# Optimization experiments

Hardware: AMD Instinct MI355X
Metric: run time of the kernel (lower is better)

## Reference

```python
import jax, jax.numpy as jnp
import numpy as np

B, N, D, H = 2, 2048, 1024, 16
DK = D // H  # 64


def setup_inputs() -> dict:
    key = jax.random.key(0)
    k0, k1, k2, k3, k4 = jax.random.split(key, 5)
    x = jax.random.normal(k0, (B, N, D), jnp.float32)
    # per-head kqv Linear weights, stored input-major: y = x @ Wkqv[h] + bkqv[h]
    Wkqv = jax.random.normal(k1, (H, D, 3 * DK), jnp.float32) / np.float32(np.sqrt(D))
    bkqv = jax.random.normal(k2, (H, 3 * DK), jnp.float32) * 0.01
    Wproj = jax.random.normal(k3, (D, D), jnp.float32) / np.float32(np.sqrt(D))
    bproj = jax.random.normal(k4, (D,), jnp.float32) * 0.01
    return {"x": x, "Wkqv": Wkqv, "bkqv": bkqv, "Wproj": Wproj, "bproj": bproj}


def reference(x, Wkqv, bkqv, Wproj, bproj):
    Bb, Nn, Dd = x.shape
    Hh, _, three_dk = Wkqv.shape
    dk = three_dk // 3
    # all-head kqv projection: [B, H, N, 3*dk]
    p = jnp.einsum('bnd,hde->bhne', x, Wkqv) + bkqv[None, :, None, :]
    # torch views (B,N,dk,3) and splits last dim -> interleaved columns
    p = p.reshape(Bb, Hh, Nn, dk, 3)
    k, q, v = p[..., 0], p[..., 1], p[..., 2]
    # NOTE: original computes attention_scores(k, q) = K @ Q^T / sqrt(dk)
    scores = jnp.einsum('bhnd,bhmd->bhnm', k, q) / jnp.sqrt(jnp.asarray(dk, x.dtype))
    causal = jnp.tril(jnp.ones((Nn, Nn), bool))  # buffer mask[-N:, -N:]
    scores = jnp.where(causal[None, None], scores, -jnp.inf)
    attn = jax.nn.softmax(scores, axis=-1)
    sa = jnp.einsum('bhnm,bhmd->bhnd', attn, v)  # [B,H,N,dk]
    sa = sa.transpose(0, 2, 1, 3).reshape(Bb, Nn, Dd)  # concat heads along feature
    return sa @ Wproj + bproj
```

## Files before the change

### kernel.cpp

```cpp
#include <hip/hip_runtime.h>
#include <hip/hip_bf16.h>


typedef __bf16 bf16x8 __attribute__((ext_vector_type(8)));
typedef float f32x4 __attribute__((ext_vector_type(4)));
typedef float f32x16 __attribute__((ext_vector_type(16)));

#define MFMA_BF16 __builtin_amdgcn_mfma_f32_16x16x32_bf16
#define MFMA32 __builtin_amdgcn_mfma_f32_32x32x16_bf16

static __device__ __forceinline__ unsigned cvtpk(float lo, float hi) {
    unsigned r;
    asm("v_cvt_pk_bf16_f32 %0, %1, %2" : "=v"(r) : "v"(lo), "v"(hi));
    return r;
}

static __device__ __forceinline__ void gld16(const void* g, void* l) {
    __builtin_amdgcn_global_load_lds(
        (const __attribute__((address_space(1))) unsigned int*)g,
        (__attribute__((address_space(3))) unsigned int*)l, 16, 0, 0);
}


__global__ __launch_bounds__(256) void cvt_f32_bf16(const float* __restrict__ in,
                                                    __hip_bfloat16* __restrict__ out) {
    int i = (blockIdx.x * 256 + threadIdx.x) * 4;
    float4 v = *(const float4*)&in[i];
    struct alignas(8) bh4 { __hip_bfloat16 a, b, c, d; };
    bh4 r{__float2bfloat16(v.x), __float2bfloat16(v.y),
          __float2bfloat16(v.z), __float2bfloat16(v.w)};
    *(bh4*)&out[i] = r;
}

__global__ __launch_bounds__(256) void transpose_cvt(const float* __restrict__ in,
                                                     __hip_bfloat16* __restrict__ out,
                                                     int R, int C) {
    __shared__ float tile[32][33];
    int b = blockIdx.z;
    int r0 = blockIdx.y * 32, c0 = blockIdx.x * 32;
    int tx = threadIdx.x, ty = threadIdx.y;
    const float* ip = in + (size_t)b * R * C;
    __hip_bfloat16* op = out + (size_t)b * R * C;
#pragma unroll
    for (int j = 0; j < 32; j += 8)
        tile[ty + j][tx] = ip[(size_t)(r0 + ty + j) * C + (c0 + tx)];
    __syncthreads();
#pragma unroll
    for (int j = 0; j < 32; j += 8)
        op[(size_t)(c0 + ty + j) * R + (r0 + tx)] = __float2bfloat16(tile[tx][ty + j]);
}

__global__ __launch_bounds__(512) void gemm_qkv(const __hip_bfloat16* __restrict__ Ag,
                                                const __hip_bfloat16* __restrict__ Btg,
                                                const float* __restrict__ bias,
                                                __hip_bfloat16* __restrict__ Kf,
                                                __hip_bfloat16* __restrict__ Qf,
                                                __hip_bfloat16* __restrict__ Vf) {
    __shared__ __hip_bfloat16 smem[57344];
    const int t = threadIdx.x;
    const int lane = t & 63, wid = t >> 6;
    const int wm = wid >> 2, wn = wid & 3;
    const int h = blockIdx.x;
    const int row0 = blockIdx.y * 256;
    const int col0 = h * 192;
    const int lr = lane & 15, lg = lane >> 4;
    const int g_r = lane >> 3;
    const int g_s8 = ((lane & 7) ^ g_r) * 8;
    const int sw0 = ((lg) ^ (lr & 7)) * 8;
    const int sw1 = ((4 + lg) ^ (lr & 7)) * 8;

#define STAGE_QKV(buf, kt)                                                            \
    do {                                                                              \
        const int k0_ = (kt) * 64;                                                    \
        __hip_bfloat16* Ad_ = smem + (buf) * 16384;                                   \
        __hip_bfloat16* Bd_ = smem + 32768 + (buf) * 12288;                           \
        _Pragma("unroll") for (int r_ = 0; r_ < 4; ++r_) {                            \
            const int grp_ = r_ * 8 + wid;                                            \
            gld16(&Ag[(size_t)(row0 + grp_ * 8 + g_r) * 1024 + k0_ + g_s8],           \
                  Ad_ + grp_ * 512);                                                  \
        }                                                                             \
        _Pragma("unroll") for (int r_ = 0; r_ < 3; ++r_) {                            \
            const int grp_ = r_ * 8 + wid;                                            \
            gld16(&Btg[(size_t)(col0 + grp_ * 8 + g_r) * 1024 + k0_ + g_s8],          \
                  Bd_ + grp_ * 512);                                                  \
        }                                                                             \
    } while (0)

    f32x4 acc[8][3] = {};

    STAGE_QKV(0, 0);
    STAGE_QKV(1, 1);
    asm volatile("s_waitcnt vmcnt(7)" ::: "memory");
    __builtin_amdgcn_sched_barrier(0);
    __builtin_amdgcn_s_barrier();
    __builtin_amdgcn_sched_barrier(0);

    int cur = 0;
    for (int kt = 0; kt < 16; ++kt) {
        const __hip_bfloat16* Ab = smem + cur * 16384;
        const __hip_bfloat16* Bb = smem + 32768 + cur * 12288;
        bf16x8 af[8], bf[3];
#pragma unroll
        for (int j = 0; j < 3; ++j)
            bf[j] = *(const bf16x8*)&Bb[(wn * 48 + j * 16 + lr) * 64 + sw0];
#pragma unroll
        for (int i = 0; i < 8; ++i)
            af[i] = *(const bf16x8*)&Ab[(wm * 128 + i * 16 + lr) * 64 + sw0];
        __builtin_amdgcn_s_setprio(1);
#pragma unroll
        for (int i = 0; i < 8; ++i)
#pragma unroll
            for (int j = 0; j < 3; ++j)
                acc[i][j] = MFMA_BF16(af[i], bf[j], acc[i][j], 0, 0, 0);
        __builtin_amdgcn_s_setprio(0);
#pragma unroll
        for (int j = 0; j < 3; ++j)
            bf[j] = *(const bf16x8*)&Bb[(wn * 48 + j * 16 + lr) * 64 + sw1];
#pragma unroll
        for (int i = 0; i < 8; ++i)
            af[i] = *(const bf16x8*)&Ab[(wm * 128 + i * 16 + lr) * 64 + sw1];
        asm volatile("s_waitcnt lgkmcnt(0)" ::: "memory");
        __builtin_amdgcn_sched_barrier(0);
        __builtin_amdgcn_s_barrier();
        __builtin_amdgcn_sched_barrier(0);
        if (kt + 2 < 16) STAGE_QKV(cur, kt + 2);
        __builtin_amdgcn_s_setprio(1);
#pragma unroll
        for (int i = 0; i < 8; ++i)
#pragma unroll
            for (int j = 0; j < 3; ++j)
                acc[i][j] = MFMA_BF16(af[i], bf[j], acc[i][j], 0, 0, 0);
        __builtin_amdgcn_s_setprio(0);
        if (kt <= 13) {
            asm volatile("s_waitcnt vmcnt(7)" ::: "memory");
        } else {
            asm volatile("s_waitcnt vmcnt(0)" ::: "memory");
        }
        __builtin_amdgcn_sched_barrier(0);
        __builtin_amdgcn_s_barrier();
        __builtin_amdgcn_sched_barrier(0);
        cur ^= 1;
    }
#undef STAGE_QKV

    const int b = row0 >> 11, n_base = row0 & 2047, bh = b * 16 + h;
    __hip_bfloat16 (*tile)[204] = (__hip_bfloat16 (*)[204])smem;
#pragma unroll
    for (int i = 0; i < 8; ++i)
#pragma unroll
        for (int j = 0; j < 3; ++j)
#pragma unroll
            for (int r = 0; r < 4; ++r) {
                int trow = wm * 128 + i * 16 + lg * 4 + r;
                int tcol = wn * 48 + j * 16 + lr;
                float v = acc[i][j][r] + bias[col0 + tcol];
                if (tcol % 3 == 0) v *= 0.125f;
                tile[trow][tcol] = __float2bfloat16(v);
            }
    __syncthreads();
#pragma unroll
    for (int k = 0; k < 4; ++k) {
        const int c = t + 512 * k;
        const int l = c & 63, lo = l & 31, hi = l >> 5;
        {
            const int dc = (c >> 6) & 3, so = c >> 8;
            ushort u[8];
#pragma unroll
            for (int i = 0; i < 8; ++i)
                u[i] = *(const ushort*)&tile[so * 32 + lo][3 * (dc * 16 + 8 * hi + i)];
            *(uint4*)&Kf[(((size_t)bh * 64 + (n_base >> 5) + so) * 4 + dc) * 512 + l * 8] =
                *(const uint4*)u;
        }
        {
            const int dc = (c >> 6) & 3, sub = (c >> 8) & 1, mt_off = c >> 9;
            ushort u[8];
#pragma unroll
            for (int i = 0; i < 8; ++i)
                u[i] = *(const ushort*)&tile[mt_off * 64 + sub * 32 + lo]
                                           [3 * (dc * 16 + 8 * hi + i) + 1];
            *(uint4*)&Qf[((((size_t)bh * 32 + (n_base >> 6) + mt_off) * 2 + sub) * 4 + dc) * 512 +
                         l * 8] = *(const uint4*)u;
        }
        {
            const int accN = (c >> 6) & 1, kc = (c >> 7) & 3, mt_off = c >> 9;
            ushort u[8];
#pragma unroll
            for (int i = 0; i < 8; ++i)
                u[i] = *(const ushort*)&tile[mt_off * 64 + kc * 16 + 8 * hi + i]
                                           [3 * (accN * 32 + lo) + 2];
            *(uint4*)&Vf[((((size_t)bh * 32 + (n_base >> 6) + mt_off) * 4 + kc) * 2 + accN) * 512 +
                         l * 8] = *(const uint4*)u;
        }
    }
}

__global__ __launch_bounds__(256, 3) void attn_fwd(const __hip_bfloat16* __restrict__ Kf,
                                                   const __hip_bfloat16* __restrict__ Qf,
                                                   const __hip_bfloat16* __restrict__ Vf,
                                                   __hip_bfloat16* __restrict__ sa) {
    __shared__ float mbuf[3][64][35];
    __shared__ __hip_bfloat16 ot[32][66];
    const int id = blockIdx.x;
    const int xcd = id & 7, qq = id >> 3;
    const int bh = xcd * 4 + (qq & 3);
    const int slice = 63 - (qq >> 2);
    const int t = threadIdx.x, lane = t & 63, wid = t >> 6;
    const int col = lane & 31, half = lane >> 5;
    const int par = wid;
    const int n0 = slice * 32;

    const __hip_bfloat16* Kfp = Kf + (size_t)bh * 131072;
    const __hip_bfloat16* Qfp = Qf + (size_t)bh * 131072;
    const __hip_bfloat16* Vfp = Vf + (size_t)bh * 131072;

    bf16x8 kf[4];
#pragma unroll
    for (int dc = 0; dc < 4; ++dc)
        kf[dc] = *(const bf16x8*)&Kfp[((size_t)slice * 4 + dc) * 512 + lane * 8];

    f32x16 acc0 = {}, acc1 = {};
    float m_run = -3.0e29f, l_run = 0.f;
    const int ng = n0 + col;
    const int T = (n0 + 95) >> 6;

    bf16x8 qa[4], qb[4];
    if (par < T) {
#pragma unroll
        for (int dc = 0; dc < 4; ++dc) {
            qa[dc] = *(const bf16x8*)&Qfp[(((size_t)par * 2 + 0) * 4 + dc) * 512 + lane * 8];
            qb[dc] = *(const bf16x8*)&Qfp[(((size_t)par * 2 + 1) * 4 + dc) * 512 + lane * 8];
        }
    }

    for (int j = par; j < T; j += 4) {
        const int m0 = j << 6;
        bf16x8 va[4], vb[4];
#pragma unroll
        for (int kc = 0; kc < 4; ++kc) {
            va[kc] = *(const bf16x8*)&Vfp[(((size_t)j * 4 + kc) * 2 + 0) * 512 + lane * 8];
            vb[kc] = *(const bf16x8*)&Vfp[(((size_t)j * 4 + kc) * 2 + 1) * 512 + lane * 8];
        }
        f32x16 s0 = {}, s1 = {};
        __builtin_amdgcn_s_setprio(1);
#pragma unroll
        for (int dc = 0; dc < 4; ++dc) s0 = MFMA32(qa[dc], kf[dc], s0, 0, 0, 0);
#pragma unroll
        for (int dc = 0; dc < 4; ++dc) s1 = MFMA32(qb[dc], kf[dc], s1, 0, 0, 0);
        __builtin_amdgcn_s_setprio(0);
        if (j + 4 < T) {
#pragma unroll
            for (int dc = 0; dc < 4; ++dc) {
                qa[dc] = *(const bf16x8*)&Qfp[(((size_t)(j + 4) * 2 + 0) * 4 + dc) * 512 + lane * 8];
                qb[dc] = *(const bf16x8*)&Qfp[(((size_t)(j + 4) * 2 + 1) * 4 + dc) * 512 + lane * 8];
            }
        }
        if (m0 + 63 > n0) {
            const int mb = m0 + 4 * half;
#pragma unroll
            for (int r = 0; r < 16; ++r) {
                int mg = mb + (r & 3) + 8 * (r >> 2);
                if (mg > ng)      s0[r] = -1e30f;
                if (mg + 32 > ng) s1[r] = -1e30f;
            }
        }
        float mx = s0[0];
#pragma unroll
        for (int r = 1; r < 16; ++r) mx = fmaxf(mx, s0[r]);
#pragma unroll
        for (int r = 0; r < 16; ++r) mx = fmaxf(mx, s1[r]);
        mx = fmaxf(mx, __shfl_xor(mx, 32));
        float nm = fmaxf(m_run, mx);
        float scale = __expf(m_run - nm);
        m_run = nm;
        float rs = 0.f;
#pragma unroll
        for (int r = 0; r < 16; ++r) { s0[r] = __expf(s0[r] - nm); rs += s0[r]; }
#pragma unroll
        for (int r = 0; r < 16; ++r) { s1[r] = __expf(s1[r] - nm); rs += s1[r]; }
        rs += __shfl_xor(rs, 32);
        l_run = l_run * scale + rs;
        acc0 *= scale;
        acc1 *= scale;

#pragma unroll
        for (int kc = 0; kc < 4; ++kc) {
            float p0, p1, p2, p3, p4, p5, p6, p7;
            if (kc == 0)      { p0=s0[0]; p1=s0[1]; p2=s0[2]; p3=s0[3]; p4=s0[4]; p5=s0[5]; p6=s0[6]; p7=s0[7]; }
            else if (kc == 1) { p0=s0[8]; p1=s0[9]; p2=s0[10]; p3=s0[11]; p4=s0[12]; p5=s0[13]; p6=s0[14]; p7=s0[15]; }
            else if (kc == 2) { p0=s1[0]; p1=s1[1]; p2=s1[2]; p3=s1[3]; p4=s1[4]; p5=s1[5]; p6=s1[6]; p7=s1[7]; }
            else              { p0=s1[8]; p1=s1[9]; p2=s1[10]; p3=s1[11]; p4=s1[12]; p5=s1[13]; p6=s1[14]; p7=s1[15]; }
            unsigned a0 = cvtpk(p0, p1), a1 = cvtpk(p2, p3);
            unsigned a2 = cvtpk(p4, p5), a3 = cvtpk(p6, p7);
            unsigned t0 = __shfl_xor(a0, 32), t1 = __shfl_xor(a1, 32);
            unsigned t2 = __shfl_xor(a2, 32), t3 = __shfl_xor(a3, 32);
            union { unsigned u[4]; bf16x8 v; } pb;
            pb.u[0] = half ? t2 : a0;
            pb.u[1] = half ? t3 : a1;
            pb.u[2] = half ? a2 : t0;
            pb.u[3] = half ? a3 : t1;
            __builtin_amdgcn_s_setprio(1);
            acc0 = MFMA32(va[kc], pb.v, acc0, 0, 0, 0);
            acc1 = MFMA32(vb[kc], pb.v, acc1, 0, 0, 0);
            __builtin_amdgcn_s_setprio(0);
        }
    }

    if (wid) {
#pragma unroll
        for (int r = 0; r < 16; ++r) {
            mbuf[wid - 1][lane][r]      = acc0[r];
            mbuf[wid - 1][lane][16 + r] = acc1[r];
        }
        mbuf[wid - 1][lane][32] = m_run;
        mbuf[wid - 1][lane][33] = l_run;
    }
    __syncthreads();
    if (!wid) {
#pragma unroll
        for (int w = 0; w < 3; ++w) {
            float mB = mbuf[w][lane][32], lB = mbuf[w][lane][33];
            float nm = fmaxf(m_run, mB);
            float sA = __expf(m_run - nm), sB = __expf(mB - nm);
            m_run = nm;
            l_run = l_run * sA + lB * sB;
#pragma unroll
            for (int r = 0; r < 16; ++r) {
                acc0[r] = acc0[r] * sA + mbuf[w][lane][r] * sB;
                acc1[r] = acc1[r] * sA + mbuf[w][lane][16 + r] * sB;
            }
        }
        float inv = 1.0f / l_run;
#pragma unroll
        for (int r = 0; r < 16; ++r) {
            int d0 = (r & 3) + 8 * (r >> 2) + 4 * half;
            ot[col][d0]      = __float2bfloat16(acc0[r] * inv);
            ot[col][32 + d0] = __float2bfloat16(acc1[r] * inv);
        }
        const int b = bh >> 4, h = bh & 15;
#pragma unroll
        for (int tt = 0; tt < 16; ++tt) {
            int rrow = tt * 2 + half;
            unsigned v = *(const unsigned*)&ot[rrow][col * 2];
            *(unsigned*)&sa[((size_t)(b * 2048 + n0 + rrow)) * 1024 + h * 64 + col * 2] = v;
        }
    }
}

__global__ __launch_bounds__(256) void gemm_proj(const __hip_bfloat16* __restrict__ Ag,
                                                 const __hip_bfloat16* __restrict__ Btg,
                                                 const float* __restrict__ bias,
                                                 float* __restrict__ out) {
    __shared__ __hip_bfloat16 smem[32768];
    const int t = threadIdx.x;
    const int lane = t & 63, wid = t >> 6;
    const int wm = wid >> 1, wn = wid & 1;
    const int row0 = blockIdx.y * 128, col0 = blockIdx.x * 128;
    const int lr = lane & 15, lg = lane >> 4;
    const int g_r = lane >> 3;
    const int g_s8 = ((lane & 7) ^ g_r) * 8;
    const int sw0 = ((lg) ^ (lr & 7)) * 8;
    const int sw1 = ((4 + lg) ^ (lr & 7)) * 8;

#define STAGE_PROJ(buf, kt)                                                           \
    do {                                                                              \
        const int k0_ = (kt) * 64;                                                    \
        __hip_bfloat16* Ad_ = smem + (buf) * 8192;                                    \
        __hip_bfloat16* Bd_ = smem + 16384 + (buf) * 8192;                            \
        _Pragma("unroll") for (int r_ = 0; r_ < 4; ++r_) {                            \
            const int grp_ = r_ * 4 + wid;                                            \
            gld16(&Ag[(size_t)(row0 + grp_ * 8 + g_r) * 1024 + k0_ + g_s8],           \
                  Ad_ + grp_ * 512);                                                  \
            gld16(&Btg[(size_t)(col0 + grp_ * 8 + g_r) * 1024 + k0_ + g_s8],          \
                  Bd_ + grp_ * 512);                                                  \
        }                                                                             \
    } while (0)

    f32x4 acc[4][4] = {};

    STAGE_PROJ(0, 0);
    STAGE_PROJ(1, 1);
    asm volatile("s_waitcnt vmcnt(8)" ::: "memory");
    __builtin_amdgcn_sched_barrier(0);
    __builtin_amdgcn_s_barrier();
    __builtin_amdgcn_sched_barrier(0);

    int cur = 0;
    for (int kt = 0; kt < 16; ++kt) {
        const __hip_bfloat16* Ab = smem + cur * 8192;
        const __hip_bfloat16* Bb = smem + 16384 + cur * 8192;
        bf16x8 af[4], bf[4];
#pragma unroll
        for (int j = 0; j < 4; ++j)
            bf[j] = *(const bf16x8*)&Bb[(wn * 64 + j * 16 + lr) * 64 + sw0];
#pragma unroll
        for (int i = 0; i < 4; ++i)
            af[i] = *(const bf16x8*)&Ab[(wm * 64 + i * 16 + lr) * 64 + sw0];
        __builtin_amdgcn_s_setprio(1);
#pragma unroll
        for (int i = 0; i < 4; ++i)
#pragma unroll
            for (int j = 0; j < 4; ++j)
                acc[i][j] = MFMA_BF16(af[i], bf[j], acc[i][j], 0, 0, 0);
        __builtin_amdgcn_s_setprio(0);
#pragma unroll
        for (int j = 0; j < 4; ++j)
            bf[j] = *(const bf16x8*)&Bb[(wn * 64 + j * 16 + lr) * 64 + sw1];
#pragma unroll
        for (int i = 0; i < 4; ++i)
            af[i] = *(const bf16x8*)&Ab[(wm * 64 + i * 16 + lr) * 64 + sw1];
        asm volatile("s_waitcnt lgkmcnt(0)" ::: "memory");
        __builtin_amdgcn_sched_barrier(0);
        __builtin_amdgcn_s_barrier();
        __builtin_amdgcn_sched_barrier(0);
        if (kt + 2 < 16) STAGE_PROJ(cur, kt + 2);
        __builtin_amdgcn_s_setprio(1);
#pragma unroll
        for (int i = 0; i < 4; ++i)
#pragma unroll
            for (int j = 0; j < 4; ++j)
                acc[i][j] = MFMA_BF16(af[i], bf[j], acc[i][j], 0, 0, 0);
        __builtin_amdgcn_s_setprio(0);
        if (kt <= 13) {
            asm volatile("s_waitcnt vmcnt(8)" ::: "memory");
        } else {
            asm volatile("s_waitcnt vmcnt(0)" ::: "memory");
        }
        __builtin_amdgcn_sched_barrier(0);
        __builtin_amdgcn_s_barrier();
        __builtin_amdgcn_sched_barrier(0);
        cur ^= 1;
    }
#undef STAGE_PROJ

#pragma unroll
    for (int i = 0; i < 4; ++i)
#pragma unroll
        for (int j = 0; j < 4; ++j)
#pragma unroll
            for (int r = 0; r < 4; ++r) {
                int rg = row0 + wm * 64 + i * 16 + lg * 4 + r;
                int cg = col0 + wn * 64 + j * 16 + lr;
                out[(size_t)rg * 1024 + cg] = acc[i][j][r] + bias[cg];
            }
}

extern "C" void kernel_launch(void* const* d_in, const int* in_sizes, int n_in,
                              void* d_out, int out_size, void* d_ws, size_t ws_size,
                              hipStream_t stream) {
    const float* x     = (const float*)d_in[0];
    const float* Wkqv  = (const float*)d_in[1];
    const float* bkqv  = (const float*)d_in[2];
    const float* Wproj = (const float*)d_in[3];
    const float* bproj = (const float*)d_in[4];

    char* w = (char*)d_ws;
    __hip_bfloat16* xb  = (__hip_bfloat16*)(w + 0);
    __hip_bfloat16* sab = (__hip_bfloat16*)(w + 0);
    __hip_bfloat16* Wt  = (__hip_bfloat16*)(w + 8388608);
    __hip_bfloat16* Kf  = (__hip_bfloat16*)(w + 16777216);
    __hip_bfloat16* Qf  = (__hip_bfloat16*)(w + 25165824);
    __hip_bfloat16* Vf  = (__hip_bfloat16*)(w + 33554432);
    __hip_bfloat16* WpT = (__hip_bfloat16*)(w + 41943040);
    if (ws_size < 50331648) return;

    cvt_f32_bf16<<<4096, 256, 0, stream>>>(x, xb);
    transpose_cvt<<<dim3(6, 32, 16), dim3(32, 8), 0, stream>>>(Wkqv, Wt, 1024, 192);
    gemm_qkv<<<dim3(16, 16), 512, 0, stream>>>(xb, Wt, bkqv, Kf, Qf, Vf);
    transpose_cvt<<<dim3(32, 32, 1), dim3(32, 8), 0, stream>>>(Wproj, WpT, 1024, 1024);
    attn_fwd<<<2048, 256, 0, stream>>>(Kf, Qf, Vf, sab);
    gemm_proj<<<dim3(8, 32), 256, 0, stream>>>(sab, WpT, bproj, (float*)d_out);
}
```

Before: 99.42 us.

## Fold log2e into K scale, seed MFMA with -m, lazy softmax rescale

Folds log2(e)/sqrt(dk) into the K projection scale so the softmax can use exp2 directly. The running max is subtracted by seeding the MFMA accumulator with -m_run. The max and sum reductions become tree reductions. Rescaling of the accumulators is skipped unless some block maximum exceeds the running max by more than a threshold of 8. This removes per-element subtracts, serial reduction chains and per-tile accumulator multiplies, at the cost of letting exponentials grow up to 2^8 before renormalisation, which is a precision risk, and of relying on an initial max of -64.

```diff
diff --git a/kernel.cpp b/kernel.cpp
--- a/kernel.cpp
+++ b/kernel.cpp
@@ -154,7 +154,7 @@
                 int trow = wm * 128 + i * 16 + lg * 4 + r;
                 int tcol = wn * 48 + j * 16 + lr;
                 float v = acc[i][j][r] + bias[col0 + tcol];
-                if (tcol % 3 == 0) v *= 0.125f;
+                if (tcol % 3 == 0) v *= 0.18033688f;
                 tile[trow][tcol] = __float2bfloat16(v);
             }
     __syncthreads();
@@ -219,7 +219,7 @@
         kf[dc] = *(const bf16x8*)&Kfp[((size_t)slice * 4 + dc) * 512 + lane * 8];
 
     f32x16 acc0 = {}, acc1 = {};
-    float m_run = -3.0e29f, l_run = 0.f;
+    float m_run = -64.0f, l_run = 0.f;
     const int ng = n0 + col;
     const int T = (n0 + 95) >> 6;
 
@@ -240,7 +240,10 @@
             va[kc] = *(const bf16x8*)&Vfp[(((size_t)j * 4 + kc) * 2 + 0) * 512 + lane * 8];
             vb[kc] = *(const bf16x8*)&Vfp[(((size_t)j * 4 + kc) * 2 + 1) * 512 + lane * 8];
         }
-        f32x16 s0 = {}, s1 = {};
+        f32x16 s0, s1;
+        const float negm = -m_run;
+#pragma unroll
+        for (int r = 0; r < 16; ++r) { s0[r] = negm; s1[r] = negm; }
         __builtin_amdgcn_s_setprio(1);
 #pragma unroll
         for (int dc = 0; dc < 4; ++dc) s0 = MFMA32(qa[dc], kf[dc], s0, 0, 0, 0);
@@ -263,24 +266,38 @@
                 if (mg + 32 > ng) s1[r] = -1e30f;
             }
         }
-        float mx = s0[0];
-#pragma unroll
-        for (int r = 1; r < 16; ++r) mx = fmaxf(mx, s0[r]);
-#pragma unroll
-        for (int r = 0; r < 16; ++r) mx = fmaxf(mx, s1[r]);
-        mx = fmaxf(mx, __shfl_xor(mx, 32));
-        float nm = fmaxf(m_run, mx);
-        float scale = __expf(m_run - nm);
-        m_run = nm;
-        float rs = 0.f;
-#pragma unroll
-        for (int r = 0; r < 16; ++r) { s0[r] = __expf(s0[r] - nm); rs += s0[r]; }
-#pragma unroll
-        for (int r = 0; r < 16; ++r) { s1[r] = __expf(s1[r] - nm); rs += s1[r]; }
-        rs += __shfl_xor(rs, 32);
-        l_run = l_run * scale + rs;
-        acc0 *= scale;
-        acc1 *= scale;
+        float mxt[16];
+#pragma unroll
+        for (int r = 0; r < 16; ++r) mxt[r] = fmaxf(s0[r], s1[r]);
+#pragma unroll
+        for (int off = 8; off; off >>= 1)
+#pragma unroll
+            for (int r = 0; r < off; ++r) mxt[r] = fmaxf(mxt[r], mxt[r + off]);
+        float mx = fmaxf(mxt[0], __shfl_xor(mxt[0], 32));
+        if (__all(mx <= 8.0f)) {
+#pragma unroll
+            for (int r = 0; r < 16; ++r) { s0[r] = exp2f(s0[r]); s1[r] = exp2f(s1[r]); }
+        } else {
+            float mxp = fmaxf(mx, 0.0f);
+            float sc = exp2f(-mxp);
+            m_run += mxp;
+            l_run *= sc;
+#pragma unroll
+            for (int r = 0; r < 16; ++r) {
+                s0[r] = exp2f(s0[r] - mxp);
+                s1[r] = exp2f(s1[r] - mxp);
+                acc0[r] *= sc;
+                acc1[r] *= sc;
+            }
+        }
+        float rst[16];
+#pragma unroll
+        for (int r = 0; r < 16; ++r) rst[r] = s0[r] + s1[r];
+#pragma unroll
+        for (int off = 8; off; off >>= 1)
+#pragma unroll
+            for (int r = 0; r < off; ++r) rst[r] += rst[r + off];
+        l_run += rst[0] + __shfl_xor(rst[0], 32);
 
 #pragma unroll
         for (int kc = 0; kc < 4; ++kc) {
@@ -320,7 +337,7 @@
         for (int w = 0; w < 3; ++w) {
             float mB = mbuf[w][lane][32], lB = mbuf[w][lane][33];
             float nm = fmaxf(m_run, mB);
-            float sA = __expf(m_run - nm), sB = __expf(mB - nm);
+            float sA = exp2f(m_run - nm), sB = exp2f(mB - nm);
             m_run = nm;
             l_run = l_run * sA + lB * sB;
 #pragma unroll
```

New measurement: 251.2 us. 2.53x slower.

## Merge prep kernels and give each attention wave its own query slice

Applied to the files above, without the earlier changes.

The x conversion and both weight transpose-converts become one launch that dispatches on block index, removing two kernel launches. The attention kernel now assigns four adjacent 32-row query slices (a band) to the four waves of one block. Each wave walks the full key range alone, and the waves stay in lockstep with a barrier so they share key/value loads in cache. This removes the cross-wave LDS merge of partial softmax states and cuts the grid from 2048 blocks to 512. In exchange each wave does serial work along the whole sequence, waves with smaller slices do redundant masked iterations up to the band maximum, and there is less parallelism per output row.

```diff
diff --git a/kernel.cpp b/kernel.cpp
--- a/kernel.cpp
+++ b/kernel.cpp
@@ -21,33 +21,48 @@
         (__attribute__((address_space(3))) unsigned int*)l, 16, 0, 0);
 }
 
-
-__global__ __launch_bounds__(256) void cvt_f32_bf16(const float* __restrict__ in,
-                                                    __hip_bfloat16* __restrict__ out) {
-    int i = (blockIdx.x * 256 + threadIdx.x) * 4;
-    float4 v = *(const float4*)&in[i];
-    struct alignas(8) bh4 { __hip_bfloat16 a, b, c, d; };
-    bh4 r{__float2bfloat16(v.x), __float2bfloat16(v.y),
-          __float2bfloat16(v.z), __float2bfloat16(v.w)};
-    *(bh4*)&out[i] = r;
-}
-
-__global__ __launch_bounds__(256) void transpose_cvt(const float* __restrict__ in,
-                                                     __hip_bfloat16* __restrict__ out,
-                                                     int R, int C) {
+__global__ __launch_bounds__(256) void prep(const float* __restrict__ x,
+                                            const float* __restrict__ Wkqv,
+                                            const float* __restrict__ Wproj,
+                                            __hip_bfloat16* __restrict__ xb,
+                                            __hip_bfloat16* __restrict__ Wt,
+                                            __hip_bfloat16* __restrict__ WpT) {
     __shared__ float tile[32][33];
-    int b = blockIdx.z;
-    int r0 = blockIdx.y * 32, c0 = blockIdx.x * 32;
-    int tx = threadIdx.x, ty = threadIdx.y;
-    const float* ip = in + (size_t)b * R * C;
-    __hip_bfloat16* op = out + (size_t)b * R * C;
+    const int bid = blockIdx.x, t = threadIdx.x;
+    if (bid < 4096) {
+        int i = (bid * 256 + t) * 4;
+        float4 v = *(const float4*)&x[i];
+        struct alignas(8) bh4 { __hip_bfloat16 a, b, c, d; };
+        bh4 r{__float2bfloat16(v.x), __float2bfloat16(v.y),
+              __float2bfloat16(v.z), __float2bfloat16(v.w)};
+        *(bh4*)&xb[i] = r;
+        return;
+    }
+    const int tx = t & 31, ty = t >> 5;
+    const float* in;
+    __hip_bfloat16* out;
+    int R, C, r0, c0;
+    if (bid < 7168) {
+        int r = bid - 4096;
+        int bz = r / 192, rem = r % 192, by = rem / 6, bx = rem % 6;
+        R = 1024; C = 192;
+        in = Wkqv + (size_t)bz * R * C;
+        out = Wt + (size_t)bz * R * C;
+        r0 = by * 32; c0 = bx * 32;
+    } else {
+        int r = bid - 7168;
+        int by = r / 32, bx = r % 32;
+        R = 1024; C = 1024;
+        in = Wproj; out = WpT;
+        r0 = by * 32; c0 = bx * 32;
+    }
 #pragma unroll
     for (int j = 0; j < 32; j += 8)
-        tile[ty + j][tx] = ip[(size_t)(r0 + ty + j) * C + (c0 + tx)];
+        tile[ty + j][tx] = in[(size_t)(r0 + ty + j) * C + (c0 + tx)];
     __syncthreads();
 #pragma unroll
     for (int j = 0; j < 32; j += 8)
-        op[(size_t)(c0 + ty + j) * R + (r0 + tx)] = __float2bfloat16(tile[tx][ty + j]);
+        out[(size_t)(c0 + ty + j) * R + (r0 + tx)] = __float2bfloat16(tile[tx][ty + j]);
 }
 
 __global__ __launch_bounds__(512) void gemm_qkv(const __hip_bfloat16* __restrict__ Ag,
@@ -198,16 +213,17 @@
                                                    const __hip_bfloat16* __restrict__ Qf,
                                                    const __hip_bfloat16* __restrict__ Vf,
                                                    __hip_bfloat16* __restrict__ sa) {
-    __shared__ float mbuf[3][64][35];
-    __shared__ __hip_bfloat16 ot[32][66];
+    __shared__ __hip_bfloat16 ot[4][32][66];
     const int id = blockIdx.x;
-    const int xcd = id & 7, qq = id >> 3;
-    const int bh = xcd * 4 + (qq & 3);
-    const int slice = 63 - (qq >> 2);
+    const int xcd = id & 7, q = id >> 3;
+    const int bh = xcd * 4 + (q & 3);
+    const int band = 15 - (q >> 2);
     const int t = threadIdx.x, lane = t & 63, wid = t >> 6;
     const int col = lane & 31, half = lane >> 5;
-    const int par = wid;
+    const int slice = band * 4 + wid;
     const int n0 = slice * 32;
+    const int ng = n0 + col;
+    const int Tmax = 2 * band + 2;
 
     const __hip_bfloat16* Kfp = Kf + (size_t)bh * 131072;
     const __hip_bfloat16* Qfp = Qf + (size_t)bh * 131072;
@@ -220,19 +236,16 @@
 
     f32x16 acc0 = {}, acc1 = {};
     float m_run = -3.0e29f, l_run = 0.f;
-    const int ng = n0 + col;
-    const int T = (n0 + 95) >> 6;
 
     bf16x8 qa[4], qb[4];
-    if (par < T) {
-#pragma unroll
-        for (int dc = 0; dc < 4; ++dc) {
-            qa[dc] = *(const bf16x8*)&Qfp[(((size_t)par * 2 + 0) * 4 + dc) * 512 + lane * 8];
-            qb[dc] = *(const bf16x8*)&Qfp[(((size_t)par * 2 + 1) * 4 + dc) * 512 + lane * 8];
-        }
-    }
-
-    for (int j = par; j < T; j += 4) {
+#pragma unroll
+    for (int dc = 0; dc < 4; ++dc) {
+        qa[dc] = *(const bf16x8*)&Qfp[((size_t)0 * 4 + dc) * 512 + lane * 8];
+        qb[dc] = *(const bf16x8*)&Qfp[((size_t)1 * 4 + dc) * 512 + lane * 8];
+    }
+
+    for (int j = 0; j < Tmax; ++j) {
+        __builtin_amdgcn_s_barrier();
         const int m0 = j << 6;
         bf16x8 va[4], vb[4];
 #pragma unroll
@@ -247,11 +260,11 @@
 #pragma unroll
         for (int dc = 0; dc < 4; ++dc) s1 = MFMA32(qb[dc], kf[dc], s1, 0, 0, 0);
         __builtin_amdgcn_s_setprio(0);
-        if (j + 4 < T) {
+        if (j + 1 < Tmax) {
 #pragma unroll
             for (int dc = 0; dc < 4; ++dc) {
-                qa[dc] = *(const bf16x8*)&Qfp[(((size_t)(j + 4) * 2 + 0) * 4 + dc) * 512 + lane * 8];
-                qb[dc] = *(const bf16x8*)&Qfp[(((size_t)(j + 4) * 2 + 1) * 4 + dc) * 512 + lane * 8];
+                qa[dc] = *(const bf16x8*)&Qfp[(((size_t)(j + 1) * 2 + 0) * 4 + dc) * 512 + lane * 8];
+                qb[dc] = *(const bf16x8*)&Qfp[(((size_t)(j + 1) * 2 + 1) * 4 + dc) * 512 + lane * 8];
             }
         }
         if (m0 + 63 > n0) {
@@ -305,44 +318,19 @@
         }
     }
 
-    if (wid) {
-#pragma unroll
-        for (int r = 0; r < 16; ++r) {
-            mbuf[wid - 1][lane][r]      = acc0[r];
-            mbuf[wid - 1][lane][16 + r] = acc1[r];
-        }
-        mbuf[wid - 1][lane][32] = m_run;
-        mbuf[wid - 1][lane][33] = l_run;
-    }
-    __syncthreads();
-    if (!wid) {
-#pragma unroll
-        for (int w = 0; w < 3; ++w) {
-            float mB = mbuf[w][lane][32], lB = mbuf[w][lane][33];
-            float nm = fmaxf(m_run, mB);
-            float sA = __expf(m_run - nm), sB = __expf(mB - nm);
-            m_run = nm;
-            l_run = l_run * sA + lB * sB;
-#pragma unroll
-            for (int r = 0; r < 16; ++r) {
-                acc0[r] = acc0[r] * sA + mbuf[w][lane][r] * sB;
-                acc1[r] = acc1[r] * sA + mbuf[w][lane][16 + r] * sB;
-            }
-        }
-        float inv = 1.0f / l_run;
-#pragma unroll
-        for (int r = 0; r < 16; ++r) {
-            int d0 = (r & 3) + 8 * (r >> 2) + 4 * half;
-            ot[col][d0]      = __float2bfloat16(acc0[r] * inv);
-            ot[col][32 + d0] = __float2bfloat16(acc1[r] * inv);
-        }
-        const int b = bh >> 4, h = bh & 15;
-#pragma unroll
-        for (int tt = 0; tt < 16; ++tt) {
-            int rrow = tt * 2 + half;
-            unsigned v = *(const unsigned*)&ot[rrow][col * 2];
-            *(unsigned*)&sa[((size_t)(b * 2048 + n0 + rrow)) * 1024 + h * 64 + col * 2] = v;
-        }
+    float inv = 1.0f / l_run;
+#pragma unroll
+    for (int r = 0; r < 16; ++r) {
+        int d0 = (r & 3) + 8 * (r >> 2) + 4 * half;
+        ot[wid][col][d0]      = __float2bfloat16(acc0[r] * inv);
+        ot[wid][col][32 + d0] = __float2bfloat16(acc1[r] * inv);
+    }
+    const int b = bh >> 4, h = bh & 15;
+#pragma unroll
+    for (int tt = 0; tt < 16; ++tt) {
+        int rrow = tt * 2 + half;
+        unsigned v = *(const unsigned*)&ot[wid][rrow][col * 2];
+        *(unsigned*)&sa[((size_t)(b * 2048 + n0 + rrow)) * 1024 + h * 64 + col * 2] = v;
     }
 }
 
@@ -463,10 +451,8 @@
     __hip_bfloat16* WpT = (__hip_bfloat16*)(w + 41943040);
     if (ws_size < 50331648) return;
 
-    cvt_f32_bf16<<<4096, 256, 0, stream>>>(x, xb);
-    transpose_cvt<<<dim3(6, 32, 16), dim3(32, 8), 0, stream>>>(Wkqv, Wt, 1024, 192);
+    prep<<<8192, 256, 0, stream>>>(x, Wkqv, Wproj, xb, Wt, WpT);
     gemm_qkv<<<dim3(16, 16), 512, 0, stream>>>(xb, Wt, bkqv, Kf, Qf, Vf);
-    transpose_cvt<<<dim3(32, 32, 1), dim3(32, 8), 0, stream>>>(Wproj, WpT, 1024, 1024);
-    attn_fwd<<<2048, 256, 0, stream>>>(Kf, Qf, Vf, sab);
+    attn_fwd<<<512, 256, 0, stream>>>(Kf, Qf, Vf, sab);
     gemm_proj<<<dim3(8, 32), 256, 0, stream>>>(sab, WpT, bproj, (float*)d_out);
 }
```

Measured after the change: 103.2 us. 1.04x slower.
